# Kernel tuning notes

Measured on AMD Instinct MI355X. Metric: run time of the kernel, lower is better.

## Reference

```python
import jax, jax.numpy as jnp
import numpy as np
from jax import lax

NB_HEADS = 8
SR_RATIO = 4
LN_EPS = 1e-6


def layer_norm(x, g, b):
    mu = jnp.mean(x, axis=-1, keepdims=True)
    var = jnp.mean(jnp.square(x - mu), axis=-1, keepdims=True)
    return (x - mu) * lax.rsqrt(var + LN_EPS) * g + b


def setup_inputs() -> dict:
    key = jax.random.key(0)
    ks = jax.random.split(key, 6)
    B, H, W, C = 16, 64, 64, 256
    N = H * W
    s = 0.02
    return {
        "x": jax.random.normal(ks[0], (B, N, C), jnp.float32),
        "q_w": jax.random.normal(ks[1], (C, C), jnp.float32) * s,
        "q_b": jnp.zeros((C,), jnp.float32),
        "kv_w": jax.random.normal(ks[2], (C, 2 * C), jnp.float32) * s,
        "kv_b": jnp.zeros((2 * C,), jnp.float32),
        "sr_w": jax.random.normal(ks[3], (SR_RATIO, SR_RATIO, C, C), jnp.float32) * s,
        "sr_b": jnp.zeros((C,), jnp.float32),
        "norm_g": jnp.ones((C,), jnp.float32),
        "norm_b": jnp.zeros((C,), jnp.float32),
        "proj_w": jax.random.normal(ks[4], (C, C), jnp.float32) * s,
        "proj_b": jnp.zeros((C,), jnp.float32),
        "grid_h": H,
        "grid_w": W,
    }


def reference(x, q_w, q_b, kv_w, kv_b, sr_w, sr_b, norm_g, norm_b, proj_w, proj_b, grid_h, grid_w):
    B, N, C = x.shape
    hd = C // NB_HEADS
    scale = hd ** (-0.5)

    # query projection -> [B, nh, N, hd]
    q = (x @ q_w + q_b).reshape(B, N, NB_HEADS, hd).transpose(0, 2, 1, 3)

    # spatial reduction: conv stride=kernel=sr_ratio on NHWC grid
    xg = x.reshape(B, grid_h, grid_w, C)
    xs = lax.conv_general_dilated(
        xg, sr_w, window_strides=(SR_RATIO, SR_RATIO), padding="VALID",
        dimension_numbers=("NHWC", "HWIO", "NHWC")) + sr_b
    M = (grid_h // SR_RATIO) * (grid_w // SR_RATIO)
    xs = layer_norm(xs.reshape(B, M, C), norm_g, norm_b)

    # key/value projection -> [B, nh, M, hd] each
    kv = (xs @ kv_w + kv_b).reshape(B, M, 2, NB_HEADS, hd).transpose(2, 0, 3, 1, 4)
    k, v = kv[0], kv[1]

    attn = jax.nn.softmax(scale * jnp.einsum("bhnd,bhmd->bhnm", q, k), axis=-1)
    out = jnp.einsum("bhnm,bhmd->bhnd", attn, v)  # [B, nh, N, hd]
    out = out.transpose(0, 2, 1, 3).reshape(B, N, C)
    return out @ proj_w + proj_b
```

## Files before the change

### kernel.cpp

```cpp
#include <hip/hip_runtime.h>
#include <math.h>

#define B_   16
#define CC   256
#define NN   4096
#define MM   256
#define NH   8
#define HD   32
#define QSCALE (0.17677669529663687f * 1.4426950408889634f)

typedef float fx4 __attribute__((ext_vector_type(4)));
typedef short sx4 __attribute__((ext_vector_type(4)));
typedef short sx8 __attribute__((ext_vector_type(8)));

__device__ inline short f2bf(float f) {
  unsigned u = __builtin_bit_cast(unsigned, f);
  u += 0x7FFFu + ((u >> 16) & 1u);
  return (short)(u >> 16);
}
__device__ inline float bf2f(short s) {
  unsigned u = ((unsigned)(unsigned short)s) << 16;
  return __builtin_bit_cast(float, u);
}
__device__ inline unsigned cvtpk_bf16(float a, float b) {
  unsigned r;
  asm("v_cvt_pk_bf16_f32 %0, %1, %2" : "=v"(r) : "v"(a), "v"(b));
  return r;
}
__device__ inline float fexp2(float x) {
#if __has_builtin(__builtin_amdgcn_exp2f)
  return __builtin_amdgcn_exp2f(x);
#else
  return exp2f(x);
#endif
}
__device__ inline float frcp(float x) {
#if __has_builtin(__builtin_amdgcn_rcpf)
  return __builtin_amdgcn_rcpf(x);
#else
  return 1.0f / x;
#endif
}

template<bool KT>
__global__ __launch_bounds__(256) void wsplit_kernel(
    const float* __restrict__ W, short* __restrict__ Th, short* __restrict__ Tl,
    int K, int N)
{
  __shared__ float Tile[64][65];
  const int t = threadIdx.x;
  const int k0 = blockIdx.y << 6, n0 = blockIdx.x << 6;
#pragma unroll
  for (int i = 0; i < 4; ++i) {
    int idx = t + (i << 8);
    int k = idx >> 4, n4 = (idx & 15) << 2;
    float4 v = *(const float4*)&W[(size_t)(k0 + k) * N + n0 + n4];
    Tile[k][n4 + 0] = v.x; Tile[k][n4 + 1] = v.y;
    Tile[k][n4 + 2] = v.z; Tile[k][n4 + 3] = v.w;
  }
  __syncthreads();
#pragma unroll
  for (int i = 0; i < 4; ++i) {
    int idx = t + (i << 8);
    int n = idx >> 4, k4 = (idx & 15) << 2;
    sx4 h, lo;
#pragma unroll
    for (int j = 0; j < 4; ++j) {
      float v = Tile[k4 + j][n];
      short hh = f2bf(v);
      h[j] = hh;
      lo[j] = f2bf(v - bf2f(hh));
    }
    int kk = k0 + k4, nn = n0 + n;
    size_t dst;
    if constexpr (KT)
      dst = ((size_t)(kk >> 5) * N << 5) + ((size_t)nn << 5) + (kk & 31);
    else
      dst = (size_t)nn * K + kk;
    *(sx4*)&Th[dst] = h;
    *(sx4*)&Tl[dst] = lo;
  }
}

template<int AM, int EP>
__global__ __launch_bounds__(256) void gemm_wide_kernel(
    const void* __restrict__ Av, const short* __restrict__ Alo,
    const short* __restrict__ Bth, const short* __restrict__ Btl,
    const float* __restrict__ bias, float* __restrict__ C,
    short* __restrict__ qout, int M, int K)
{
  __shared__ short Bhs[256][36];
  __shared__ short Bls[256][36];
  const int t = threadIdx.x;
  const int bm = blockIdx.x << 6;
  const int w = t >> 6, l = t & 63, g = l >> 4, c = l & 15;
  const int g8 = g << 3;
  const int arow = bm + (w << 4) + c;
  const int srow = t >> 2;
  const int skc  = (t & 3) << 3;

  sx8 pb0h, pb1h, pb2h, pb3h, pb0l, pb1l, pb2l, pb3l;
  auto LOADB = [&](int k0) {
    const size_t tb = ((size_t)(k0 >> 5) << 13) + ((size_t)t << 3);
    pb0h = *(const sx8*)&Bth[tb];         pb1h = *(const sx8*)&Bth[tb + 2048];
    pb2h = *(const sx8*)&Bth[tb + 4096];  pb3h = *(const sx8*)&Bth[tb + 6144];
    pb0l = *(const sx8*)&Btl[tb];         pb1l = *(const sx8*)&Btl[tb + 2048];
    pb2l = *(const sx8*)&Btl[tb + 4096];  pb3l = *(const sx8*)&Btl[tb + 6144];
  };

  float4 pa0, pa1; sx8 pah, pal;
  auto LOADA = [&](int k0) {
    if constexpr (AM == 2) {
      size_t idx = ((size_t)(arow >> 12) << 20) + ((size_t)(k0 >> 5) << 17)
                 + ((size_t)(arow & 4095) << 5) + g8;
      pah = *(const sx8*)&((const short*)Av)[idx];
      pal = *(const sx8*)&Alo[idx];
    } else {
      const float* ap = (const float*)Av + (size_t)arow * K + k0 + g8;
      pa0 = *(const float4*)ap;
      pa1 = *(const float4*)(ap + 4);
    }
  };

  fx4 acc[16];
#pragma unroll
  for (int j = 0; j < 16; ++j) acc[j] = fx4{0.f, 0.f, 0.f, 0.f};

  LOADB(0); LOADA(0);
  for (int k0 = 0; k0 < K; k0 += 32) {
    *(sx8*)&Bhs[srow][skc]       = pb0h;
    *(sx8*)&Bhs[64 + srow][skc]  = pb1h;
    *(sx8*)&Bhs[128 + srow][skc] = pb2h;
    *(sx8*)&Bhs[192 + srow][skc] = pb3h;
    *(sx8*)&Bls[srow][skc]       = pb0l;
    *(sx8*)&Bls[64 + srow][skc]  = pb1l;
    *(sx8*)&Bls[128 + srow][skc] = pb2l;
    *(sx8*)&Bls[192 + srow][skc] = pb3l;
    sx8 ah, al;
    if constexpr (AM == 2) { ah = pah; al = pal; }
    else {
      ah[0]=f2bf(pa0.x); al[0]=f2bf(pa0.x-bf2f(ah[0]));
      ah[1]=f2bf(pa0.y); al[1]=f2bf(pa0.y-bf2f(ah[1]));
      ah[2]=f2bf(pa0.z); al[2]=f2bf(pa0.z-bf2f(ah[2]));
      ah[3]=f2bf(pa0.w); al[3]=f2bf(pa0.w-bf2f(ah[3]));
      ah[4]=f2bf(pa1.x); al[4]=f2bf(pa1.x-bf2f(ah[4]));
      ah[5]=f2bf(pa1.y); al[5]=f2bf(pa1.y-bf2f(ah[5]));
      ah[6]=f2bf(pa1.z); al[6]=f2bf(pa1.z-bf2f(ah[6]));
      ah[7]=f2bf(pa1.w); al[7]=f2bf(pa1.w-bf2f(ah[7]));
    }
    __syncthreads();
    if (k0 + 32 < K) { LOADB(k0 + 32); LOADA(k0 + 32); }
#pragma unroll
    for (int j = 0; j < 16; ++j) {
      sx8 bh = *(const sx8*)&Bhs[(j << 4) + c][g8];
      sx8 bl = *(const sx8*)&Bls[(j << 4) + c][g8];
      acc[j] = __builtin_amdgcn_mfma_f32_16x16x32_bf16(ah, bh, acc[j], 0, 0, 0);
      acc[j] = __builtin_amdgcn_mfma_f32_16x16x32_bf16(al, bh, acc[j], 0, 0, 0);
      acc[j] = __builtin_amdgcn_mfma_f32_16x16x32_bf16(ah, bl, acc[j], 0, 0, 0);
    }
    __syncthreads();
  }

  const int orow = bm + (w << 4) + (g << 2);
#pragma unroll
  for (int j = 0; j < 16; ++j) {
    const int col = (j << 4) + c;
    const float bb = bias[col];
    if constexpr (EP == 0) {
#pragma unroll
      for (int i = 0; i < 4; ++i)
        C[(size_t)(orow + i) * 256 + col] = acc[j][i] + bb;
    } else {
      const int h = col >> 5, d = col & 31;
#pragma unroll
      for (int i = 0; i < 4; ++i) {
        int r = orow + i;
        qout[((size_t)(((r >> 12) << 3) + h) * 4096 + (r & 4095)) * 32 + d]
            = f2bf((acc[j][i] + bb) * QSCALE);
      }
    }
  }
}

template<bool GATHER, int EPI>
__global__ __launch_bounds__(256) void gemm_split_kernel(
    const float* __restrict__ A, const short* __restrict__ Bth,
    const short* __restrict__ Btl, const float* __restrict__ bias,
    float* __restrict__ C, short* __restrict__ kout, short* __restrict__ vout,
    int M, int N, int K)
{
  __shared__ short Ah[64][40], Al[64][40], Bh[64][40], Bl[64][40];
  const int t = threadIdx.x;
  const int bm = blockIdx.y << 6, bn = blockIdx.x << 6;
  const int ar = t >> 2, ak = (t & 3) << 3;
  const int bc = t >> 2, bk = (t & 3) << 3;

  int sp_base = 0;
  if (GATHER) {
    int gr = bm + ar;
    int b = gr >> 8, mm2 = gr & 255;
    int oh = mm2 >> 4, ow = mm2 & 15;
    sp_base = b * 4096 + oh * 256 + ow * 4;
  }
  const size_t brow = (size_t)(bn + bc) * K;

  const int KS = K / gridDim.z;
  const int kbeg = blockIdx.z * KS, kend = kbeg + KS;

  float4 pa0, pa1; sx8 pbh, pbl;
  auto LOADG = [&](int k0) {
    int k = k0 + ak;
    const float* ap;
    if (GATHER) {
      int pos = k >> 8, ci = k & 255;
      ap = &A[(size_t)(sp_base + ((pos >> 2) << 6) + (pos & 3)) * 256 + ci];
    } else {
      ap = &A[(size_t)(bm + ar) * K + k];
    }
    pa0 = *(const float4*)ap;
    pa1 = *(const float4*)(ap + 4);
    pbh = *(const sx8*)&Bth[brow + k0 + bk];
    pbl = *(const sx8*)&Btl[brow + k0 + bk];
  };

  const int w = t >> 6, l = t & 63, g = l >> 4, c = l & 15;
  const int wr = w >> 1, wc = w & 1;
  const int ra0 = (wr << 5) + c, ra1 = ra0 + 16;
  const int cb0 = (wc << 5) + c, cb1 = cb0 + 16;
  const int g8 = g << 3;

  fx4 acc00 = {0.f,0.f,0.f,0.f}, acc01 = acc00, acc10 = acc00, acc11 = acc00;

  LOADG(kbeg);
  for (int k0 = kbeg; k0 < kend; k0 += 32) {
    sx4 AH0, AL0, AH1, AL1;
    AH0[0]=f2bf(pa0.x); AL0[0]=f2bf(pa0.x-bf2f(AH0[0]));
    AH0[1]=f2bf(pa0.y); AL0[1]=f2bf(pa0.y-bf2f(AH0[1]));
    AH0[2]=f2bf(pa0.z); AL0[2]=f2bf(pa0.z-bf2f(AH0[2]));
    AH0[3]=f2bf(pa0.w); AL0[3]=f2bf(pa0.w-bf2f(AH0[3]));
    AH1[0]=f2bf(pa1.x); AL1[0]=f2bf(pa1.x-bf2f(AH1[0]));
    AH1[1]=f2bf(pa1.y); AL1[1]=f2bf(pa1.y-bf2f(AH1[1]));
    AH1[2]=f2bf(pa1.z); AL1[2]=f2bf(pa1.z-bf2f(AH1[2]));
    AH1[3]=f2bf(pa1.w); AL1[3]=f2bf(pa1.w-bf2f(AH1[3]));
    *(sx4*)&Ah[ar][ak]     = AH0;  *(sx4*)&Ah[ar][ak + 4] = AH1;
    *(sx4*)&Al[ar][ak]     = AL0;  *(sx4*)&Al[ar][ak + 4] = AL1;
    *(sx8*)&Bh[bc][bk] = pbh;      *(sx8*)&Bl[bc][bk] = pbl;
    __syncthreads();
    if (k0 + 32 < kend) LOADG(k0 + 32);

    sx8 a0h = *(const sx8*)&Ah[ra0][g8];
    sx8 a0l = *(const sx8*)&Al[ra0][g8];
    sx8 a1h = *(const sx8*)&Ah[ra1][g8];
    sx8 a1l = *(const sx8*)&Al[ra1][g8];
    sx8 b0h = *(const sx8*)&Bh[cb0][g8];
    sx8 b0l = *(const sx8*)&Bl[cb0][g8];
    sx8 b1h = *(const sx8*)&Bh[cb1][g8];
    sx8 b1l = *(const sx8*)&Bl[cb1][g8];

    acc00 = __builtin_amdgcn_mfma_f32_16x16x32_bf16(a0h, b0h, acc00, 0, 0, 0);
    acc01 = __builtin_amdgcn_mfma_f32_16x16x32_bf16(a0h, b1h, acc01, 0, 0, 0);
    acc10 = __builtin_amdgcn_mfma_f32_16x16x32_bf16(a1h, b0h, acc10, 0, 0, 0);
    acc11 = __builtin_amdgcn_mfma_f32_16x16x32_bf16(a1h, b1h, acc11, 0, 0, 0);
    acc00 = __builtin_amdgcn_mfma_f32_16x16x32_bf16(a0l, b0h, acc00, 0, 0, 0);
    acc01 = __builtin_amdgcn_mfma_f32_16x16x32_bf16(a0l, b1h, acc01, 0, 0, 0);
    acc10 = __builtin_amdgcn_mfma_f32_16x16x32_bf16(a1l, b0h, acc10, 0, 0, 0);
    acc11 = __builtin_amdgcn_mfma_f32_16x16x32_bf16(a1l, b1h, acc11, 0, 0, 0);
    acc00 = __builtin_amdgcn_mfma_f32_16x16x32_bf16(a0h, b0l, acc00, 0, 0, 0);
    acc01 = __builtin_amdgcn_mfma_f32_16x16x32_bf16(a0h, b1l, acc01, 0, 0, 0);
    acc10 = __builtin_amdgcn_mfma_f32_16x16x32_bf16(a1h, b0l, acc10, 0, 0, 0);
    acc11 = __builtin_amdgcn_mfma_f32_16x16x32_bf16(a1h, b1l, acc11, 0, 0, 0);
    __syncthreads();
  }

  const int col0 = bn + (wc << 5);
  const int row0 = bm + (wr << 5) + (g << 2);
  if constexpr (EPI == 1) {
    float* Cz = C + (size_t)blockIdx.z * M * N;
#pragma unroll
    for (int i = 0; i < 4; ++i) {
      Cz[(size_t)(row0 + i) * N + col0 + c]           = acc00[i];
      Cz[(size_t)(row0 + i) * N + col0 + 16 + c]      = acc01[i];
      Cz[(size_t)(row0 + 16 + i) * N + col0 + c]      = acc10[i];
      Cz[(size_t)(row0 + 16 + i) * N + col0 + 16 + c] = acc11[i];
    }
  } else {
    const float b0 = bias[col0 + c], b1 = bias[col0 + 16 + c];
    auto emit = [&](int row, int n, float v) {
      int b = row >> 8, m = row & 255;
      short* dst = (n < 256) ? kout : vout;
      int nn = n & 255;
      int h = nn >> 5, d = nn & 31;
      dst[(size_t)(((b << 3) + h) * 256 + m) * 32 + d] = f2bf(v);
    };
#pragma unroll
    for (int i = 0; i < 4; ++i) {
      emit(row0 + i,      col0 + c,      acc00[i] + b0);
      emit(row0 + i,      col0 + 16 + c, acc01[i] + b1);
      emit(row0 + 16 + i, col0 + c,      acc10[i] + b0);
      emit(row0 + 16 + i, col0 + 16 + c, acc11[i] + b1);
    }
  }
}

__global__ __launch_bounds__(256) void ln_reduce_kernel(
    const float* __restrict__ parts, const float* __restrict__ bias,
    const float* __restrict__ g, const float* __restrict__ bta,
    float* __restrict__ xs)
{
  const int row = blockIdx.x, t = threadIdx.x;
  const size_t MN = (size_t)4096 * 256;
  const size_t off = (size_t)row * CC + t;
  float v = bias[t];
#pragma unroll
  for (int p = 0; p < 8; ++p) v += parts[p * MN + off];
  float s = v, s2 = v * v;
#pragma unroll
  for (int offs = 32; offs; offs >>= 1) {
    s  += __shfl_xor(s,  offs, 64);
    s2 += __shfl_xor(s2, offs, 64);
  }
  __shared__ float red[8];
  const int w = t >> 6, lane = t & 63;
  if (lane == 0) { red[w] = s; red[4 + w] = s2; }
  __syncthreads();
  float ts  = red[0] + red[1] + red[2] + red[3];
  float ts2 = red[4] + red[5] + red[6] + red[7];
  float mu  = ts * (1.0f / 256.0f);
  float var = ts2 * (1.0f / 256.0f) - mu * mu;
  float o = (v - mu) * rsqrtf(var + 1e-6f) * g[t] + bta[t];
  xs[off] = o;
}

__global__ __launch_bounds__(256, 3) void attn_mfma8_kernel(
    short* __restrict__ qob, short* __restrict__ olo,
    const short* __restrict__ kbf, const short* __restrict__ vbf)
{
  __shared__ short Vt[32 * 264];
  __shared__ short Ps[4 * 16 * 264];

  const int tid = threadIdx.x;
  const int bid = blockIdx.x;
  const int nt = bid & 63, h = (bid >> 6) & 7, b = bid >> 9;
  const int n0 = nt << 6;
  const int bh = (b << 3) + h;
  const short* kb = kbf + (size_t)bh * 8192;
  const short* vb = vbf + (size_t)bh * 8192;

  {
    const int msrc = ((tid & 15) << 4) | (tid >> 4);
    sx8 v0 = *(const sx8*)&vb[msrc * 32 + 0];
    sx8 v1 = *(const sx8*)&vb[msrc * 32 + 8];
    sx8 v2 = *(const sx8*)&vb[msrc * 32 + 16];
    sx8 v3 = *(const sx8*)&vb[msrc * 32 + 24];
#pragma unroll
    for (int e = 0; e < 8; ++e) {
      Vt[(e)      * 264 + tid] = v0[e];
      Vt[(8 + e)  * 264 + tid] = v1[e];
      Vt[(16 + e) * 264 + tid] = v2[e];
      Vt[(24 + e) * 264 + tid] = v3[e];
    }
  }

  const int w = tid >> 6, l = tid & 63;
  const int g = l >> 4, c = l & 15;

  sx8 aq = *(const sx8*)&qob[((size_t)bh * 4096 + n0 + w * 16 + c) * 32 + (g << 3)];

  fx4 acc[16];
#pragma unroll
  for (int j = 0; j < 16; ++j) {
    sx8 bk = *(const sx8*)&kb[(j * 16 + c) * 32 + (g << 3)];
    fx4 z = {0.f, 0.f, 0.f, 0.f};
    acc[j] = __builtin_amdgcn_mfma_f32_16x16x32_bf16(aq, bk, z, 0, 0, 0);
  }

#pragma unroll
  for (int j = 0; j < 16; ++j) {
#pragma unroll
    for (int i = 0; i < 4; ++i) acc[j][i] = fexp2(acc[j][i]);
  }

  const int pbase = (w << 4) * 264;
#pragma unroll
  for (int i = 0; i < 4; ++i) {
    unsigned p0 = cvtpk_bf16(acc[0][i],  acc[1][i]);
    unsigned p1 = cvtpk_bf16(acc[2][i],  acc[3][i]);
    unsigned p2 = cvtpk_bf16(acc[4][i],  acc[5][i]);
    unsigned p3 = cvtpk_bf16(acc[6][i],  acc[7][i]);
    unsigned p4 = cvtpk_bf16(acc[8][i],  acc[9][i]);
    unsigned p5 = cvtpk_bf16(acc[10][i], acc[11][i]);
    unsigned p6 = cvtpk_bf16(acc[12][i], acc[13][i]);
    unsigned p7 = cvtpk_bf16(acc[14][i], acc[15][i]);
    unsigned* dst = (unsigned*)&Ps[pbase + ((g << 2) + i) * 264 + (c << 4)];
    uint4 lo4; lo4.x = p0; lo4.y = p1; lo4.z = p2; lo4.w = p3;
    uint4 hi4; hi4.x = p4; hi4.y = p5; hi4.z = p6; hi4.w = p7;
    *(uint4*)dst       = lo4;
    *(uint4*)(dst + 4) = hi4;
  }

  __syncthreads();

  const short onebf = (short)0x3F80;
  sx8 ones = { onebf, onebf, onebf, onebf, onebf, onebf, onebf, onebf };
  fx4 o0 = {0.f,0.f,0.f,0.f}, o1 = o0, o2 = o0;
#pragma unroll
  for (int s = 0; s < 8; ++s) {
    sx8 ap  = *(const sx8*)&Ps[pbase + c * 264 + (s << 5) + (g << 3)];
    sx8 bv0 = *(const sx8*)&Vt[(c)      * 264 + (s << 5) + (g << 3)];
    sx8 bv1 = *(const sx8*)&Vt[(16 + c) * 264 + (s << 5) + (g << 3)];
    o0 = __builtin_amdgcn_mfma_f32_16x16x32_bf16(ap, bv0, o0, 0, 0, 0);
    o1 = __builtin_amdgcn_mfma_f32_16x16x32_bf16(ap, bv1, o1, 0, 0, 0);
    o2 = __builtin_amdgcn_mfma_f32_16x16x32_bf16(ap, ones, o2, 0, 0, 0);
  }

#pragma unroll
  for (int i = 0; i < 4; ++i) {
    float inv = frcp(o2[i]);
    int n = n0 + w * 16 + (g << 2) + i;
    size_t base = ((size_t)bh * 4096 + n) * 32;
    float v0 = o0[i] * inv, v1 = o1[i] * inv;
    short h0 = f2bf(v0), h1 = f2bf(v1);
    qob[base + c]      = h0;  olo[base + c]      = f2bf(v0 - bf2f(h0));
    qob[base + 16 + c] = h1;  olo[base + 16 + c] = f2bf(v1 - bf2f(h1));
  }
}

extern "C" void kernel_launch(void* const* d_in, const int* in_sizes, int n_in,
                              void* d_out, int out_size, void* d_ws, size_t ws_size,
                              hipStream_t stream) {
  const float* x      = (const float*)d_in[0];
  const float* q_w    = (const float*)d_in[1];
  const float* q_b    = (const float*)d_in[2];
  const float* kv_w   = (const float*)d_in[3];
  const float* kv_b   = (const float*)d_in[4];
  const float* sr_w   = (const float*)d_in[5];
  const float* sr_b   = (const float*)d_in[6];
  const float* norm_g = (const float*)d_in[7];
  const float* norm_b = (const float*)d_in[8];
  const float* proj_w = (const float*)d_in[9];
  const float* proj_b = (const float*)d_in[10];
  float* out = (float*)d_out;

  float* xsbuf = (float*)d_ws;
  short* qbf   = (short*)(xsbuf + 1048576);
  short* olo   = qbf + 16777216;
  short* kbf   = olo + 16777216;
  short* vbf   = kbf + 2097152;
  short* qwt_h  = vbf + 2097152;
  short* qwt_l  = qwt_h + 65536;
  short* kvwt_h = qwt_l + 65536;
  short* kvwt_l = kvwt_h + 131072;
  short* pwt_h  = kvwt_l + 131072;
  short* pwt_l  = pwt_h + 65536;
  short* swt_h  = pwt_l + 65536;
  short* swt_l  = swt_h + 1048576;
  float* partf = out;

  dim3 blk(256);

  wsplit_kernel<true><<<dim3(CC/64, CC/64), blk, 0, stream>>>(q_w, qwt_h, qwt_l, CC, CC);
  wsplit_kernel<false><<<dim3(2*CC/64, CC/64), blk, 0, stream>>>(kv_w, kvwt_h, kvwt_l, CC, 2*CC);
  wsplit_kernel<true><<<dim3(CC/64, CC/64), blk, 0, stream>>>(proj_w, pwt_h, pwt_l, CC, CC);
  wsplit_kernel<false><<<dim3(CC/64, 4096/64), blk, 0, stream>>>(sr_w, swt_h, swt_l, 4096, CC);

  gemm_wide_kernel<0,3><<<dim3((B_*NN)/64), blk, 0, stream>>>(
      x, nullptr, qwt_h, qwt_l, q_b, nullptr, qbf, B_*NN, CC);

  gemm_split_kernel<true,1><<<dim3(CC/64, (B_*MM)/64, 8), blk, 0, stream>>>(
      x, swt_h, swt_l, sr_b, partf, nullptr, nullptr, B_*MM, CC, 4096);

  ln_reduce_kernel<<<B_ * MM, blk, 0, stream>>>(partf, sr_b, norm_g, norm_b, xsbuf);

  gemm_split_kernel<false,2><<<dim3((2*CC)/64, (B_*MM)/64, 1), blk, 0, stream>>>(
      xsbuf, kvwt_h, kvwt_l, kv_b, nullptr, kbf, vbf, B_*MM, 2*CC, CC);

  attn_mfma8_kernel<<<B_ * NH * (NN / 64), blk, 0, stream>>>(qbf, olo, kbf, vbf);

  gemm_wide_kernel<2,0><<<dim3((B_*NN)/64), blk, 0, stream>>>(
      qbf, olo, pwt_h, pwt_l, proj_b, out, nullptr, B_*NN, CC);
}
```

Measured before the change: 216.6 us.

## Remap wide GEMM warps to column slices and drop shared-memory B staging

The wide GEMM (used for the Q projection and the output projection) is re-tiled. Each warp now covers all 64 rows of the block and its own 64-column slice, instead of 16 rows by all 256 columns. B fragments are loaded straight from global memory into registers, which removes the shared-memory tiles and both __syncthreads per k-step. Every thread now loads and converts four A row fragments instead of one, so A global traffic and fp32-to-bf16 split work per block are roughly quadrupled. In exchange B reuse across rows comes from registers, with no LDS round trip.

```diff
diff --git a/kernel.cpp b/kernel.cpp
--- a/kernel.cpp
+++ b/kernel.cpp
@@ -83,100 +83,128 @@
 }
 
 template<int AM, int EP>
-__global__ __launch_bounds__(256) void gemm_wide_kernel(
+__global__ __launch_bounds__(256) void gemm_wide3_kernel(
     const void* __restrict__ Av, const short* __restrict__ Alo,
     const short* __restrict__ Bth, const short* __restrict__ Btl,
     const float* __restrict__ bias, float* __restrict__ C,
     short* __restrict__ qout, int M, int K)
 {
-  __shared__ short Bhs[256][36];
-  __shared__ short Bls[256][36];
   const int t = threadIdx.x;
   const int bm = blockIdx.x << 6;
   const int w = t >> 6, l = t & 63, g = l >> 4, c = l & 15;
   const int g8 = g << 3;
-  const int arow = bm + (w << 4) + c;
-  const int srow = t >> 2;
-  const int skc  = (t & 3) << 3;
-
-  sx8 pb0h, pb1h, pb2h, pb3h, pb0l, pb1l, pb2l, pb3l;
+  const int colbase = w << 6;
+
+  sx8 pbh0, pbh1, pbh2, pbh3, pbl0, pbl1, pbl2, pbl3;
   auto LOADB = [&](int k0) {
-    const size_t tb = ((size_t)(k0 >> 5) << 13) + ((size_t)t << 3);
-    pb0h = *(const sx8*)&Bth[tb];         pb1h = *(const sx8*)&Bth[tb + 2048];
-    pb2h = *(const sx8*)&Bth[tb + 4096];  pb3h = *(const sx8*)&Bth[tb + 6144];
-    pb0l = *(const sx8*)&Btl[tb];         pb1l = *(const sx8*)&Btl[tb + 2048];
-    pb2l = *(const sx8*)&Btl[tb + 4096];  pb3l = *(const sx8*)&Btl[tb + 6144];
+    const short* bh_ = Bth + (((size_t)(k0 >> 5)) << 13) + (colbase + c) * 32 + g8;
+    const short* bl_ = Btl + (((size_t)(k0 >> 5)) << 13) + (colbase + c) * 32 + g8;
+    pbh0 = *(const sx8*)&bh_[0];    pbl0 = *(const sx8*)&bl_[0];
+    pbh1 = *(const sx8*)&bh_[512];  pbl1 = *(const sx8*)&bl_[512];
+    pbh2 = *(const sx8*)&bh_[1024]; pbl2 = *(const sx8*)&bl_[1024];
+    pbh3 = *(const sx8*)&bh_[1536]; pbl3 = *(const sx8*)&bl_[1536];
   };
 
-  float4 pa0, pa1; sx8 pah, pal;
+  float4 pa00, pa01, pa10, pa11, pa20, pa21, pa30, pa31;
+  sx8 pah0, pah1, pah2, pah3, pal0_, pal1_, pal2_, pal3_;
   auto LOADA = [&](int k0) {
     if constexpr (AM == 2) {
-      size_t idx = ((size_t)(arow >> 12) << 20) + ((size_t)(k0 >> 5) << 17)
-                 + ((size_t)(arow & 4095) << 5) + g8;
-      pah = *(const sx8*)&((const short*)Av)[idx];
-      pal = *(const sx8*)&Alo[idx];
+#pragma unroll
+      for (int rr = 0; rr < 4; ++rr) {
+        int arow = bm + (rr << 4) + c;
+        size_t idx = ((size_t)(arow >> 12) << 20) + ((size_t)(k0 >> 5) << 17)
+                   + ((size_t)(arow & 4095) << 5) + g8;
+        sx8 hv = *(const sx8*)&((const short*)Av)[idx];
+        sx8 lv = *(const sx8*)&Alo[idx];
+        if (rr == 0) { pah0 = hv; pal0_ = lv; }
+        else if (rr == 1) { pah1 = hv; pal1_ = lv; }
+        else if (rr == 2) { pah2 = hv; pal2_ = lv; }
+        else { pah3 = hv; pal3_ = lv; }
+      }
     } else {
-      const float* ap = (const float*)Av + (size_t)arow * K + k0 + g8;
-      pa0 = *(const float4*)ap;
-      pa1 = *(const float4*)(ap + 4);
+#pragma unroll
+      for (int rr = 0; rr < 4; ++rr) {
+        int arow = bm + (rr << 4) + c;
+        const float* ap = (const float*)Av + (size_t)arow * K + k0 + g8;
+        float4 v0 = *(const float4*)ap;
+        float4 v1 = *(const float4*)(ap + 4);
+        if (rr == 0) { pa00 = v0; pa01 = v1; }
+        else if (rr == 1) { pa10 = v0; pa11 = v1; }
+        else if (rr == 2) { pa20 = v0; pa21 = v1; }
+        else { pa30 = v0; pa31 = v1; }
+      }
     }
   };
 
   fx4 acc[16];
 #pragma unroll
   for (int j = 0; j < 16; ++j) acc[j] = fx4{0.f, 0.f, 0.f, 0.f};
+
+  auto CVT = [&](float4 a0, float4 a1, sx8& h, sx8& lo) {
+    h[0]=f2bf(a0.x); lo[0]=f2bf(a0.x-bf2f(h[0]));
+    h[1]=f2bf(a0.y); lo[1]=f2bf(a0.y-bf2f(h[1]));
+    h[2]=f2bf(a0.z); lo[2]=f2bf(a0.z-bf2f(h[2]));
+    h[3]=f2bf(a0.w); lo[3]=f2bf(a0.w-bf2f(h[3]));
+    h[4]=f2bf(a1.x); lo[4]=f2bf(a1.x-bf2f(h[4]));
+    h[5]=f2bf(a1.y); lo[5]=f2bf(a1.y-bf2f(h[5]));
+    h[6]=f2bf(a1.z); lo[6]=f2bf(a1.z-bf2f(h[6]));
+    h[7]=f2bf(a1.w); lo[7]=f2bf(a1.w-bf2f(h[7]));
+  };
 
   LOADB(0); LOADA(0);
   for (int k0 = 0; k0 < K; k0 += 32) {
-    *(sx8*)&Bhs[srow][skc]       = pb0h;
-    *(sx8*)&Bhs[64 + srow][skc]  = pb1h;
-    *(sx8*)&Bhs[128 + srow][skc] = pb2h;
-    *(sx8*)&Bhs[192 + srow][skc] = pb3h;
-    *(sx8*)&Bls[srow][skc]       = pb0l;
-    *(sx8*)&Bls[64 + srow][skc]  = pb1l;
-    *(sx8*)&Bls[128 + srow][skc] = pb2l;
-    *(sx8*)&Bls[192 + srow][skc] = pb3l;
-    sx8 ah, al;
-    if constexpr (AM == 2) { ah = pah; al = pal; }
-    else {
-      ah[0]=f2bf(pa0.x); al[0]=f2bf(pa0.x-bf2f(ah[0]));
-      ah[1]=f2bf(pa0.y); al[1]=f2bf(pa0.y-bf2f(ah[1]));
-      ah[2]=f2bf(pa0.z); al[2]=f2bf(pa0.z-bf2f(ah[2]));
-      ah[3]=f2bf(pa0.w); al[3]=f2bf(pa0.w-bf2f(ah[3]));
-      ah[4]=f2bf(pa1.x); al[4]=f2bf(pa1.x-bf2f(ah[4]));
-      ah[5]=f2bf(pa1.y); al[5]=f2bf(pa1.y-bf2f(ah[5]));
-      ah[6]=f2bf(pa1.z); al[6]=f2bf(pa1.z-bf2f(ah[6]));
-      ah[7]=f2bf(pa1.w); al[7]=f2bf(pa1.w-bf2f(ah[7]));
-    }
-    __syncthreads();
+    sx8 bh0 = pbh0, bh1 = pbh1, bh2 = pbh2, bh3 = pbh3;
+    sx8 bl0 = pbl0, bl1 = pbl1, bl2 = pbl2, bl3 = pbl3;
+    sx8 ah0, ah1, ah2, ah3, al0, al1, al2, al3;
+    if constexpr (AM == 2) {
+      ah0 = pah0; al0 = pal0_; ah1 = pah1; al1 = pal1_;
+      ah2 = pah2; al2 = pal2_; ah3 = pah3; al3 = pal3_;
+    } else {
+      CVT(pa00, pa01, ah0, al0); CVT(pa10, pa11, ah1, al1);
+      CVT(pa20, pa21, ah2, al2); CVT(pa30, pa31, ah3, al3);
+    }
     if (k0 + 32 < K) { LOADB(k0 + 32); LOADA(k0 + 32); }
-#pragma unroll
-    for (int j = 0; j < 16; ++j) {
-      sx8 bh = *(const sx8*)&Bhs[(j << 4) + c][g8];
-      sx8 bl = *(const sx8*)&Bls[(j << 4) + c][g8];
-      acc[j] = __builtin_amdgcn_mfma_f32_16x16x32_bf16(ah, bh, acc[j], 0, 0, 0);
-      acc[j] = __builtin_amdgcn_mfma_f32_16x16x32_bf16(al, bh, acc[j], 0, 0, 0);
-      acc[j] = __builtin_amdgcn_mfma_f32_16x16x32_bf16(ah, bl, acc[j], 0, 0, 0);
-    }
-    __syncthreads();
-  }
-
-  const int orow = bm + (w << 4) + (g << 2);
-#pragma unroll
-  for (int j = 0; j < 16; ++j) {
-    const int col = (j << 4) + c;
+
+#define STEP(jj, BH, BL) \
+    acc[0*4+jj] = __builtin_amdgcn_mfma_f32_16x16x32_bf16(ah0, BH, acc[0*4+jj], 0, 0, 0); \
+    acc[1*4+jj] = __builtin_amdgcn_mfma_f32_16x16x32_bf16(ah1, BH, acc[1*4+jj], 0, 0, 0); \
+    acc[2*4+jj] = __builtin_amdgcn_mfma_f32_16x16x32_bf16(ah2, BH, acc[2*4+jj], 0, 0, 0); \
+    acc[3*4+jj] = __builtin_amdgcn_mfma_f32_16x16x32_bf16(ah3, BH, acc[3*4+jj], 0, 0, 0); \
+    acc[0*4+jj] = __builtin_amdgcn_mfma_f32_16x16x32_bf16(al0, BH, acc[0*4+jj], 0, 0, 0); \
+    acc[1*4+jj] = __builtin_amdgcn_mfma_f32_16x16x32_bf16(al1, BH, acc[1*4+jj], 0, 0, 0); \
+    acc[2*4+jj] = __builtin_amdgcn_mfma_f32_16x16x32_bf16(al2, BH, acc[2*4+jj], 0, 0, 0); \
+    acc[3*4+jj] = __builtin_amdgcn_mfma_f32_16x16x32_bf16(al3, BH, acc[3*4+jj], 0, 0, 0); \
+    acc[0*4+jj] = __builtin_amdgcn_mfma_f32_16x16x32_bf16(ah0, BL, acc[0*4+jj], 0, 0, 0); \
+    acc[1*4+jj] = __builtin_amdgcn_mfma_f32_16x16x32_bf16(ah1, BL, acc[1*4+jj], 0, 0, 0); \
+    acc[2*4+jj] = __builtin_amdgcn_mfma_f32_16x16x32_bf16(ah2, BL, acc[2*4+jj], 0, 0, 0); \
+    acc[3*4+jj] = __builtin_amdgcn_mfma_f32_16x16x32_bf16(ah3, BL, acc[3*4+jj], 0, 0, 0);
+
+    STEP(0, bh0, bl0)
+    STEP(1, bh1, bl1)
+    STEP(2, bh2, bl2)
+    STEP(3, bh3, bl3)
+#undef STEP
+  }
+
+#pragma unroll
+  for (int jj = 0; jj < 4; ++jj) {
+    const int col = colbase + (jj << 4) + c;
     const float bb = bias[col];
-    if constexpr (EP == 0) {
-#pragma unroll
-      for (int i = 0; i < 4; ++i)
-        C[(size_t)(orow + i) * 256 + col] = acc[j][i] + bb;
-    } else {
-      const int h = col >> 5, d = col & 31;
-#pragma unroll
-      for (int i = 0; i < 4; ++i) {
-        int r = orow + i;
-        qout[((size_t)(((r >> 12) << 3) + h) * 4096 + (r & 4095)) * 32 + d]
-            = f2bf((acc[j][i] + bb) * QSCALE);
+#pragma unroll
+    for (int rr = 0; rr < 4; ++rr) {
+      const int orow = bm + (rr << 4) + (g << 2);
+      if constexpr (EP == 0) {
+#pragma unroll
+        for (int i = 0; i < 4; ++i)
+          C[(size_t)(orow + i) * 256 + col] = acc[(rr << 2) + jj][i] + bb;
+      } else {
+        const int h = col >> 5, d = col & 31;
+#pragma unroll
+        for (int i = 0; i < 4; ++i) {
+          int r = orow + i;
+          qout[((size_t)(((r >> 12) << 3) + h) * 4096 + (r & 4095)) * 32 + d]
+              = f2bf((acc[(rr << 2) + jj][i] + bb) * QSCALE);
+        }
       }
     }
   }
@@ -463,7 +491,7 @@
   wsplit_kernel<true><<<dim3(CC/64, CC/64), blk, 0, stream>>>(proj_w, pwt_h, pwt_l, CC, CC);
   wsplit_kernel<false><<<dim3(CC/64, 4096/64), blk, 0, stream>>>(sr_w, swt_h, swt_l, 4096, CC);
 
-  gemm_wide_kernel<0,3><<<dim3((B_*NN)/64), blk, 0, stream>>>(
+  gemm_wide3_kernel<0,3><<<dim3((B_*NN)/64), blk, 0, stream>>>(
       x, nullptr, qwt_h, qwt_l, q_b, nullptr, qbf, B_*NN, CC);
 
   gemm_split_kernel<true,1><<<dim3(CC/64, (B_*MM)/64, 8), blk, 0, stream>>>(
@@ -476,6 +504,6 @@
 
   attn_mfma8_kernel<<<B_ * NH * (NN / 64), blk, 0, stream>>>(qbf, olo, kbf, vbf);
 
-  gemm_wide_kernel<2,0><<<dim3((B_*NN)/64), blk, 0, stream>>>(
+  gemm_wide3_kernel<2,0><<<dim3((B_*NN)/64), blk, 0, stream>>>(
       qbf, olo, pwt_h, pwt_l, proj_b, out, nullptr, B_*NN, CC);
 }
```

After: 231.0 us. +6.6%, slower.
